# Kernel tuning notes

Measured on AMD Instinct MI355X. Metric: run time of the kernel, lower is better.

Reference implementation:

```python
import jax, jax.numpy as jnp
import numpy as np

B, T, C, L = 1024, 256, 100, 64  # batch, time steps, classes (blank=C-1), label length
NEG = -1e30   # safe -inf for log-space DP
EPS = 1e-7    # Keras K.epsilon() added before log


def setup_inputs() -> dict:
    key = jax.random.key(0)
    k1, k2 = jax.random.split(key)
    logits = jax.random.normal(k1, (B, T, C), dtype=jnp.float32)
    y_pred = jax.nn.softmax(logits, axis=-1)  # ctc_batch_cost expects probabilities
    y_true = jax.random.randint(k2, (B, L), 0, C - 1)  # labels in [0, C-2]; blank=C-1
    return {"y_true": y_true, "y_pred": y_pred}


def ctc_loss(y_true, y_pred):
    """Faithful K.ctc_batch_cost with full input/label lengths, blank = C-1."""
    Bb, Tt, Cc = y_pred.shape
    Ll = y_true.shape[1]
    S = 2 * Ll + 1  # extended label lattice: blank-interleaved
    blank = Cc - 1

    # extended labels: [blank, l0, blank, l1, ..., blank]
    ext = jnp.full((Bb, S), blank, dtype=y_true.dtype).at[:, 1::2].set(y_true)
    # skip-transition allowed when ext[s] is non-blank and differs from ext[s-2]
    ext_m2 = jnp.concatenate([jnp.full((Bb, 2), -1, ext.dtype), ext[:, :-2]], axis=1)
    allow = (ext != blank) & (ext != ext_m2)  # [B,S]

    logp = jnp.log(y_pred + EPS)  # [B,T,C]
    # gather log-probs on the lattice once: [B,T,S]
    lp_ext = jnp.take_along_axis(
        logp, jnp.broadcast_to(ext[:, None, :], (Bb, Tt, S)), axis=2)
    lp_seq = jnp.moveaxis(lp_ext, 1, 0)  # [T,B,S] for scan

    # alpha init: only states 0 (blank) and 1 (first label) reachable at t=0
    alpha0 = jnp.where(jnp.arange(S)[None, :] < 2, lp_seq[0], NEG)

    def shift(a, k):
        return jnp.concatenate(
            [jnp.full((Bb, k), NEG, a.dtype), a[:, :-k]], axis=1)

    def step(alpha, lp_t):
        new = jnp.logaddexp(
            jnp.logaddexp(alpha, shift(alpha, 1)),
            jnp.where(allow, shift(alpha, 2), NEG)) + lp_t
        return new, None

    alphaT, _ = jax.lax.scan(step, alpha0, lp_seq[1:])
    # total prob = alpha[T-1, S-1] + alpha[T-1, S-2]
    loss = -jnp.logaddexp(alphaT[:, -1], alphaT[:, -2])
    return loss[:, None]  # ctc_batch_cost returns shape [B,1]


def reference(y_true, y_pred):
    return ctc_loss(y_true, y_pred)
```

## Files before the change

kernel.cpp:

```cpp
#include <hip/hip_runtime.h>

#define B_ 1024
#define T_ 256
#define C_ 100
#define L_ 64
#define EPS_ 1e-7f
#define LN2 0.69314718055994530942f

#define CH 8
#define NCH (T_ / CH)
#define DEPTH 3

#define LOG2F(x) __builtin_amdgcn_logf(x)

typedef const __attribute__((address_space(1))) void GV;
typedef __attribute__((address_space(3))) void LV;

__device__ __forceinline__ void gload_lds4(const void* g, void* l) {
    __builtin_amdgcn_global_load_lds((GV*)g, (LV*)l, 4, 0, 0);
}

__device__ __forceinline__ float dpp_shr1(float x) {
    return __int_as_float(__builtin_amdgcn_update_dpp(
        0, __float_as_int(x), 0x138, 0xf, 0xf, false));
}

#define STEP(pb_, pl_) do {                                               \
    const float up1 = dpp_shr1(a1);                                       \
    const float s   = allow ? up1 : 0.0f;                                 \
    const float n0  = (a0 + up1) * (pb_);                                 \
    const float n1  = ((a1 + a0) + s) * (pl_);                            \
    const float n2  = (a2 + a1) * (pb_);                                  \
    a0 = n0; a1 = n1; a2 = n2;                                            \
} while (0)

#define PLAN() do {                                                       \
    float m_ = fmaxf(fmaxf(a0, a1), a2);                                  \
    _Pragma("unroll")                                                     \
    for (int d_ = 1; d_ < 64; d_ <<= 1) m_ = fmaxf(m_, __shfl_xor(m_, d_)); \
    const int e_ = (__float_as_int(m_) >> 23) & 255;                      \
    rs_K = 127 - e_;                                                      \
    rs_scale = __int_as_float((254 - e_) << 23);           \
} while (0)

#define APPLY() do { a0 *= rs_scale; a1 *= rs_scale; a2 *= rs_scale;      \
                     Sacc += rs_K; } while (0)

#define ISSUE(c_) do {                                                    \
    const int bufi_ = (c_) & 3;                                           \
    _Pragma("unroll")                                                     \
    for (int j_ = 0; j_ < CH; ++j_)                                       \
        gload_lds4(pL + ((c_) * CH + j_) * C_, &plbuf[bufi_][j_][0]);     \
    gload_lds4(pBl + (c_) * CH * C_, &pbbuf[bufi_][0]);                   \
} while (0)

__global__ __launch_bounds__(64) void ctc_kernel(
    const int* __restrict__ y_true,
    const float* __restrict__ y_pred,
    float* __restrict__ out)
{
    __shared__ float plbuf[4][CH][64];
    __shared__ float pbbuf[4][64];

    const int b    = blockIdx.x;
    const int lane = threadIdx.x;

    const float* __restrict__ base = y_pred + (size_t)b * T_ * C_;
    const int label   = y_true[b * L_ + lane];
    const int labprev = __shfl_up(label, 1);
    const bool allow  = (lane == 0) || (label != labprev);

    const float* __restrict__ pL  = base + label;
    const float* __restrict__ pBl = base + (C_ - 1) + (lane & (CH - 1)) * C_;

    ISSUE(0); ISSUE(1); ISSUE(2);

    float a0 = 0.0f, a1 = 0.0f, a2 = 0.0f;
    float rs_scale = 1.0f;
    int   rs_K = 0, Sacc = 0;

    #pragma unroll
    for (int c = 0; c < NCH; ++c) {
        if (c <= NCH - 3)      { asm volatile("s_waitcnt vmcnt(18)" ::: "memory"); }
        else if (c == NCH - 2) { asm volatile("s_waitcnt vmcnt(9)"  ::: "memory"); }
        else                   { asm volatile("s_waitcnt vmcnt(0)"  ::: "memory"); }

        const int bufi = c & 3;
        if (c == 0) {
            a0 = (lane == 0) ? (pbbuf[0][0] + EPS_) : 0.0f;
            a1 = (lane == 0) ? (plbuf[0][0][lane] + EPS_) : 0.0f;
            a2 = 0.0f;
            PLAN();
            #pragma unroll
            for (int j = 1; j < CH; ++j)
                STEP(pbbuf[bufi][j] + EPS_, plbuf[bufi][j][lane] + EPS_);
        } else {
            APPLY();
            PLAN();
            #pragma unroll
            for (int j = 0; j < CH; ++j)
                STEP(pbbuf[bufi][j] + EPS_, plbuf[bufi][j][lane] + EPS_);
        }

        if (c + DEPTH < NCH) ISSUE(c + DEPTH);
    }

    if (lane == 63) {
        out[b] = -LN2 * (LOG2F(a1 + a2) - (float)Sacc);
    }
}

extern "C" void kernel_launch(void* const* d_in, const int* in_sizes, int n_in,
                              void* d_out, int out_size, void* d_ws, size_t ws_size,
                              hipStream_t stream) {
    const int*   y_true = (const int*)d_in[0];
    const float* y_pred = (const float*)d_in[1];
    float*       out    = (float*)d_out;

    ctc_kernel<<<dim3(B_), dim3(64), 0, stream>>>(y_true, y_pred, out);
}
```

Baseline: 24.01 us.

## Split CTC recursion into forward and backward waves meeting at midpoint

Each block now runs two waves. One computes the forward alpha recursion over the first half of the time steps, the other computes the backward beta recursion over the second half, and the results are combined with a dot product at the midpoint through LDS. This halves the serial dependency chain per batch element, which dominates latency. The prefetch depth grows from 3 to 6 chunks with 8-slot LDS buffers. The cost is a doubled block size, more LDS per block, and a more complex combine with separate exponent-scale accumulators.

```diff
diff --git a/kernel.cpp b/kernel.cpp
--- a/kernel.cpp
+++ b/kernel.cpp
@@ -8,8 +8,8 @@
 #define LN2 0.69314718055994530942f
 
 #define CH 8
-#define NCH (T_ / CH)
-#define DEPTH 3
+#define NCH 16
+#define DEPTH 6
 
 #define LOG2F(x) __builtin_amdgcn_logf(x)
 
@@ -24,8 +24,24 @@
     return __int_as_float(__builtin_amdgcn_update_dpp(
         0, __float_as_int(x), 0x138, 0xf, 0xf, false));
 }
-
-#define STEP(pb_, pl_) do {                                               \
+__device__ __forceinline__ float dpp_shl1(float x) {
+    return __int_as_float(__builtin_amdgcn_update_dpp(
+        0, __float_as_int(x), 0x130, 0xf, 0xf, false));
+}
+
+#define PLAN(x0_, x1_, x2_) do {                                          \
+    float m_ = fmaxf(fmaxf(x0_, x1_), x2_);                               \
+    _Pragma("unroll")                                                     \
+    for (int d_ = 1; d_ < 64; d_ <<= 1) m_ = fmaxf(m_, __shfl_xor(m_, d_)); \
+    const int e_ = (__float_as_int(m_) >> 23) & 255;                      \
+    rs_K = 127 - e_;                                                      \
+    rs_scale = __int_as_float((254 - e_) << 23);           \
+} while (0)
+
+#define APPLY(x0_, x1_, x2_) do { x0_ *= rs_scale; x1_ *= rs_scale;       \
+    x2_ *= rs_scale; Sacc += rs_K; } while (0)
+
+#define FSTEP(pb_, pl_) do {                                              \
     const float up1 = dpp_shr1(a1);                                       \
     const float s   = allow ? up1 : 0.0f;                                 \
     const float n0  = (a0 + up1) * (pb_);                                 \
@@ -34,79 +50,143 @@
     a0 = n0; a1 = n1; a2 = n2;                                            \
 } while (0)
 
-#define PLAN() do {                                                       \
-    float m_ = fmaxf(fmaxf(a0, a1), a2);                                  \
-    _Pragma("unroll")                                                     \
-    for (int d_ = 1; d_ < 64; d_ <<= 1) m_ = fmaxf(m_, __shfl_xor(m_, d_)); \
-    const int e_ = (__float_as_int(m_) >> 23) & 255;                      \
-    rs_K = 127 - e_;                                                      \
-    rs_scale = __int_as_float((254 - e_) << 23);           \
-} while (0)
-
-#define APPLY() do { a0 *= rs_scale; a1 *= rs_scale; a2 *= rs_scale;      \
-                     Sacc += rs_K; } while (0)
-
-#define ISSUE(c_) do {                                                    \
-    const int bufi_ = (c_) & 3;                                           \
+#define BSTEP(pb_, pl_) do {                                              \
+    const float db0 = dpp_shl1(a0);                                       \
+    const float db1 = dpp_shl1(a1);                                       \
+    const float sc0 = is63 ? a2 : db0;                                    \
+    const float sk  = allowN ? db1 : 0.0f;    \
+    const float n0  = (a0 + a1) * (pb_);                                  \
+    const float n1  = ((a1 + sc0) + sk) * (pl_);                          \
+    const float n2  = a2 * (pb_);                                         \
+    a0 = n0; a1 = n1; a2 = n2;                                            \
+} while (0)
+
+#define WAIT_CHUNK(c_) do {                                               \
+    const int n_ = 9 * ((NCH - 1 - (c_)) < (DEPTH - 1) ? (NCH - 1 - (c_)) \
+                                                       : (DEPTH - 1));    \
+    switch (n_) {                                                         \
+    case 45: asm volatile("s_waitcnt vmcnt(45)" ::: "memory"); break;     \
+    case 36: asm volatile("s_waitcnt vmcnt(36)" ::: "memory"); break;     \
+    case 27: asm volatile("s_waitcnt vmcnt(27)" ::: "memory"); break;     \
+    case 18: asm volatile("s_waitcnt vmcnt(18)" ::: "memory"); break;     \
+    case  9: asm volatile("s_waitcnt vmcnt(9)"  ::: "memory"); break;     \
+    default: asm volatile("s_waitcnt vmcnt(0)"  ::: "memory"); break;     \
+    }                                                                     \
+} while (0)
+
+#define ISSUE(wv_, c_, toff_expr, boff_expr) do {                         \
     _Pragma("unroll")                                                     \
     for (int j_ = 0; j_ < CH; ++j_)                                       \
-        gload_lds4(pL + ((c_) * CH + j_) * C_, &plbuf[bufi_][j_][0]);     \
-    gload_lds4(pBl + (c_) * CH * C_, &pbbuf[bufi_][0]);                   \
-} while (0)
-
-__global__ __launch_bounds__(64) void ctc_kernel(
+        gload_lds4(pL + (toff_expr) * C_, &plbuf[wv_][(c_) & 7][j_][0]);  \
+    gload_lds4(pBlane + (boff_expr) * C_, &pbbuf[wv_][(c_) & 7][0]);      \
+} while (0)
+
+__global__ __launch_bounds__(128) void ctc_kernel(
     const int* __restrict__ y_true,
     const float* __restrict__ y_pred,
     float* __restrict__ out)
 {
-    __shared__ float plbuf[4][CH][64];
-    __shared__ float pbbuf[4][64];
-
+    __shared__ float plbuf[2][8][CH][64];
+    __shared__ float pbbuf[2][8][64];
+    __shared__ float sG0[64], sG1[64];
+    __shared__ float sG2;
+    __shared__ int   sSaccB;
+
+    const int tid  = threadIdx.x;
+    const int lane = tid & 63;
+    const int wv   = tid >> 6;
     const int b    = blockIdx.x;
-    const int lane = threadIdx.x;
 
     const float* __restrict__ base = y_pred + (size_t)b * T_ * C_;
-    const int label   = y_true[b * L_ + lane];
-    const int labprev = __shfl_up(label, 1);
-    const bool allow  = (lane == 0) || (label != labprev);
-
-    const float* __restrict__ pL  = base + label;
-    const float* __restrict__ pBl = base + (C_ - 1) + (lane & (CH - 1)) * C_;
-
-    ISSUE(0); ISSUE(1); ISSUE(2);
+    const int  label   = y_true[b * L_ + lane];
+    const int  labprev = __shfl_up(label, 1);
+    const bool allow   = (lane == 0) || (label != labprev);
+    const bool is63    = (lane == 63);
+    const bool allowN  = (bool)__shfl_down((int)allow, 1);
+
+    const float* __restrict__ pL = base + label;
 
     float a0 = 0.0f, a1 = 0.0f, a2 = 0.0f;
     float rs_scale = 1.0f;
     int   rs_K = 0, Sacc = 0;
 
-    #pragma unroll
-    for (int c = 0; c < NCH; ++c) {
-        if (c <= NCH - 3)      { asm volatile("s_waitcnt vmcnt(18)" ::: "memory"); }
-        else if (c == NCH - 2) { asm volatile("s_waitcnt vmcnt(9)"  ::: "memory"); }
-        else                   { asm volatile("s_waitcnt vmcnt(0)"  ::: "memory"); }
-
-        const int bufi = c & 3;
-        if (c == 0) {
-            a0 = (lane == 0) ? (pbbuf[0][0] + EPS_) : 0.0f;
-            a1 = (lane == 0) ? (plbuf[0][0][lane] + EPS_) : 0.0f;
-            a2 = 0.0f;
-            PLAN();
-            #pragma unroll
-            for (int j = 1; j < CH; ++j)
-                STEP(pbbuf[bufi][j] + EPS_, plbuf[bufi][j][lane] + EPS_);
-        } else {
-            APPLY();
-            PLAN();
-            #pragma unroll
-            for (int j = 0; j < CH; ++j)
-                STEP(pbbuf[bufi][j] + EPS_, plbuf[bufi][j][lane] + EPS_);
+    if (wv == 0) {
+        const float* __restrict__ pBlane = base + (C_ - 1) + (lane & 7) * C_;
+        #pragma unroll
+        for (int c = 0; c < DEPTH; ++c) ISSUE(0, c, c * CH + j_, c * CH);
+
+        #pragma unroll
+        for (int c = 0; c < NCH; ++c) {
+            WAIT_CHUNK(c);
+            const int bi = c & 7;
+            if (c == 0) {
+                a0 = (lane == 0) ? (pbbuf[0][0][0] + EPS_) : 0.0f;
+                a1 = (lane == 0) ? (plbuf[0][0][0][lane] + EPS_) : 0.0f;
+                a2 = 0.0f;
+                PLAN(a0, a1, a2);
+                #pragma unroll
+                for (int j = 1; j < CH; ++j)
+                    FSTEP(pbbuf[0][bi][j] + EPS_, plbuf[0][bi][j][lane] + EPS_);
+            } else {
+                APPLY(a0, a1, a2);
+                PLAN(a0, a1, a2);
+                #pragma unroll
+                for (int j = 0; j < CH; ++j)
+                    FSTEP(pbbuf[0][bi][j] + EPS_, plbuf[0][bi][j][lane] + EPS_);
+            }
+            if (c + DEPTH < NCH) ISSUE(0, c + DEPTH, (c + DEPTH) * CH + j_, (c + DEPTH) * CH);
         }
 
-        if (c + DEPTH < NCH) ISSUE(c + DEPTH);
+        APPLY(a0, a1, a2);
+        PLAN(a0, a1, a2);
+        APPLY(a0, a1, a2);
+    } else {
+        const float* __restrict__ pBlane = base + (C_ - 1) + (T_ - 1 - (lane & 7)) * C_;
+        #pragma unroll
+        for (int c = 0; c < DEPTH; ++c) ISSUE(1, c, T_ - 1 - (c * CH + j_), -(c * CH));
+
+        #pragma unroll
+        for (int c = 0; c < NCH; ++c) {
+            WAIT_CHUNK(c);
+            const int bi = c & 7;
+            if (c == 0) {
+                a2 = pbbuf[1][0][0] + EPS_;
+                a1 = is63 ? (plbuf[1][0][0][lane] + EPS_) : 0.0f;
+                a0 = 0.0f;
+                PLAN(a0, a1, a2);
+                #pragma unroll
+                for (int j = 1; j < CH; ++j)
+                    BSTEP(pbbuf[1][bi][j] + EPS_, plbuf[1][bi][j][lane] + EPS_);
+            } else {
+                APPLY(a0, a1, a2);
+                PLAN(a0, a1, a2);
+                #pragma unroll
+                for (int j = 0; j < CH; ++j)
+                    BSTEP(pbbuf[1][bi][j] + EPS_, plbuf[1][bi][j][lane] + EPS_);
+            }
+            if (c + DEPTH < NCH) ISSUE(1, c + DEPTH, T_ - 1 - ((c + DEPTH) * CH + j_), -((c + DEPTH) * CH));
+        }
+
+        APPLY(a0, a1, a2);
+        PLAN(a0, a1, a2);
+        APPLY(a0, a1, a2);
+
+        const float db0 = dpp_shl1(a0);
+        const float db1 = dpp_shl1(a1);
+        sG0[lane] = a0 + a1;
+        sG1[lane] = a1 + (is63 ? a2 : db0) + (allowN ? db1 : 0.0f);
+        if (is63) { sG2 = a2; sSaccB = Sacc; }
     }
 
-    if (lane == 63) {
-        out[b] = -LN2 * (LOG2F(a1 + a2) - (float)Sacc);
+    __syncthreads();
+
+    if (wv == 0) {
+        float prod = a0 * sG0[lane] + a1 * sG1[lane];
+        if (is63) prod += a2 * sG2;
+        #pragma unroll
+        for (int d = 1; d < 64; d <<= 1) prod += __shfl_xor(prod, d);
+        if (lane == 0)
+            out[b] = -LN2 * (LOG2F(prod) - (float)(Sacc + sSaccB));
     }
 }
 
@@ -117,5 +197,5 @@
     const float* y_pred = (const float*)d_in[1];
     float*       out    = (float*)d_out;
 
-    ctc_kernel<<<dim3(B_), dim3(64), 0, stream>>>(y_true, y_pred, out);
-}
+    ctc_kernel<<<dim3(B_), dim3(128), 0, stream>>>(y_true, y_pred, out);
+}
```

New measurement: 24.51 us. 1.02x slower.
